# Performance work log

Hardware: AMD Instinct MI355X
Metric: run time of the kernel (lower is better)

## Reference

```python
import jax, jax.numpy as jnp
import numpy as np

KNN_K = 16
EPS = 1e-5


def _knn_idx(p, k):
    # p: [B,3,N] -> idx [B,N,k] of nearest neighbors (self excluded)
    pt = jnp.swapaxes(p, 1, 2)                      # [B,N,3]
    xx = jnp.sum(pt * pt, axis=-1)                  # [B,N]
    inner = jnp.einsum('bnd,bmd->bnm', pt, pt)      # [B,N,N]
    dist = -(xx[:, :, None] - 2.0 * inner + xx[:, None, :])  # -||pi-pj||^2
    N = pt.shape[1]
    dist = dist - 1e9 * jnp.eye(N, dtype=dist.dtype)
    return jax.lax.top_k(dist, k)[1]


def _ln(x, g, b):
    mu = jnp.mean(x, axis=-1, keepdims=True)
    var = jnp.mean((x - mu) ** 2, axis=-1, keepdims=True)
    return (x - mu) * jax.lax.rsqrt(var + EPS) * g + b


_gather = jax.vmap(lambda a, i: a[i])  # a:[N,C], i:[N,k] -> [N,k,C]


def setup_inputs() -> dict:
    key = jax.random.key(0)
    ks = jax.random.split(key, 24)
    Cin, C, B, N = 64, 128, 8, 2048
    s = lambda k_, shp, fan: jax.random.normal(k_, shp, jnp.float32) * (1.0 / np.sqrt(fan))
    return {
        'x': jax.random.normal(ks[0], (B, Cin, N), jnp.float32),
        'p': jax.random.normal(ks[1], (B, 3, N), jnp.float32),
        'Win': s(ks[2], (C, Cin), Cin), 'bin_': jnp.zeros((C,), jnp.float32),
        'Wq': s(ks[3], (C, C), C), 'Wk': s(ks[4], (C, C), C), 'Wv': s(ks[5], (C, C), C),
        'Wd1': s(ks[6], (C, 3), 3), 'bd1': jnp.zeros((C,), jnp.float32),
        'Wd2': s(ks[7], (C, C), C), 'bd2': jnp.zeros((C,), jnp.float32),
        'Wa': s(ks[8], (C, C), C), 'ba': jnp.zeros((C,), jnp.float32),
        'g1': jnp.ones((C,), jnp.float32), 'b1': jnp.zeros((C,), jnp.float32),
        'g2': jnp.ones((C,), jnp.float32), 'b2': jnp.zeros((C,), jnp.float32),
        'Wf1': s(ks[9], (4 * C, C), C), 'bf1': jnp.zeros((4 * C,), jnp.float32),
        'Wf2': s(ks[10], (C, 4 * C), 4 * C), 'bf2': jnp.zeros((C,), jnp.float32),
    }


def reference(x, p, Win, bin_, Wq, Wk, Wv, Wd1, bd1, Wd2, bd2, Wa, ba,
              g1, b1, g2, b2, Wf1, bf1, Wf2, bf2) -> jnp.ndarray:
    B, _, N = x.shape
    k = min(KNN_K, max(1, N - 1))
    # in_proj (conv1x1 == per-point linear); work in [B,N,C]
    h = jnp.einsum('oc,bcn->bno', Win, x) + bin_          # [B,N,C]
    hn = _ln(h, g1, b1)
    idx = _knn_idx(p, k)                                  # [B,N,k] (int)
    q = hn @ Wq.T                                         # [B,N,C]
    k_all = hn @ Wk.T
    v_all = hn @ Wv.T
    k_j = _gather(k_all, idx)                             # [B,N,k,C]
    v_j = _gather(v_all, idx)
    pt = jnp.swapaxes(p, 1, 2)                            # [B,N,3]
    p_j = _gather(pt, idx)                                # [B,N,k,3]
    rel = pt[:, :, None, :] - p_j                         # [B,N,k,3]
    d = jax.nn.relu(rel @ Wd1.T + bd1) @ Wd2.T + bd2      # [B,N,k,C]
    logits = (q[:, :, None, :] - k_j + d) @ Wa.T + ba     # [B,N,k,C]
    a = jax.nn.softmax(logits, axis=2)                    # softmax over neighbors
    y = jnp.sum(a * (v_j + d), axis=2)                    # [B,N,C]
    h = h + y
    h2 = _ln(h, g2, b2)
    h = h + jax.nn.relu(h2 @ Wf1.T + bf1) @ Wf2.T + bf2
    return jnp.swapaxes(h, 1, 2)                          # [B,C,N]
```

## Files before the change

### kernel.cpp

```cpp
#include <hip/hip_runtime.h>

typedef __bf16 bf16_t;
typedef __bf16 bf16x8 __attribute__((ext_vector_type(8)));
typedef __bf16 bf16x2 __attribute__((ext_vector_type(2)));
typedef float  f32x4  __attribute__((ext_vector_type(4)));

#define MFMA16(a,b,c) __builtin_amdgcn_mfma_f32_16x16x32_bf16((a),(b),(c),0,0,0)

#define BB 8
#define NN 2048
#define CC 128
#define CIN 64
#define KNB 16
#define BNT (BB*NN)

static __device__ __forceinline__ int remap256(int x) { return ((x & 7) << 5) | (x >> 3); }

static __device__ __forceinline__ bf16x8 cvt8(const float* src) {
  f32x4 a0 = *(const f32x4*)src;
  f32x4 a1 = *(const f32x4*)(src + 4);
  bf16x8 fr;
  fr[0] = (__bf16)a0[0]; fr[1] = (__bf16)a0[1]; fr[2] = (__bf16)a0[2]; fr[3] = (__bf16)a0[3];
  fr[4] = (__bf16)a1[0]; fr[5] = (__bf16)a1[1]; fr[6] = (__bf16)a1[2]; fr[7] = (__bf16)a1[3];
  return fr;
}

__global__ __launch_bounds__(256) void compw_k(
    const float* __restrict__ Wa, const float* __restrict__ Wq,
    const float* __restrict__ Wk, const float* __restrict__ Wd2,
    const float* __restrict__ ba, const float* __restrict__ bd2,
    float* __restrict__ Waq, float* __restrict__ Wak, float* __restrict__ Wda,
    float* __restrict__ cb) {
  __shared__ float Bs[64 * 128];
  int t = threadIdx.x;
  int mat = blockIdx.y;
  const float* B = mat == 0 ? Wq : mat == 1 ? Wk : Wd2;
  float* O = mat == 0 ? Waq : mat == 1 ? Wak : Wda;
  int row = blockIdx.x * 16 + (t >> 4);
  int c0 = (t & 15) * 8;
  const float* ar = Wa + row * 128;
  float acc[8] = {};
  for (int half = 0; half < 2; ++half) {
    __syncthreads();
    for (int i = t; i < 64 * 128 / 4; i += 256)
      ((f32x4*)Bs)[i] = ((const f32x4*)(B + half * 64 * 128))[i];
    __syncthreads();
    #pragma unroll 4
    for (int e = 0; e < 64; ++e) {
      float av = ar[half * 64 + e];
      #pragma unroll
      for (int j = 0; j < 8; ++j) acc[j] = fmaf(av, Bs[e * 128 + c0 + j], acc[j]);
    }
  }
  #pragma unroll
  for (int j = 0; j < 8; ++j) O[row * 128 + c0 + j] = acc[j];
  if (mat == 2 && blockIdx.x == 0 && t < 128) {
    float s = 0.f;
    for (int e = 0; e < 128; ++e) s = fmaf(Wa[t * 128 + e], bd2[e], s);
    cb[t] = ba[t] + s;
  }
}

__global__ __launch_bounds__(256) void inproj_ln_k(
    const float* __restrict__ x, const float* __restrict__ Win, const float* __restrict__ bin,
    const float* __restrict__ g1, const float* __restrict__ b1,
    float* __restrict__ h, bf16_t* __restrict__ hnb) {
  __shared__ bf16_t As[64 * 72];
  __shared__ bf16_t Bs[128 * 72];
  __shared__ float hs[64 * 132];
  int t = threadIdx.x;
  int lane = t & 63, w = t >> 6, quad = lane >> 4, l15 = lane & 15;
  int mBase = remap256(blockIdx.x) * 64;
  int b = mBase >> 11, n0 = mBase & (NN - 1);
  const float* xb = x + (size_t)b * CIN * NN;
  {
    int k = t >> 2, part = t & 3;
    #pragma unroll
    for (int i = 0; i < 4; ++i) {
      f32x4 v = *(const f32x4*)(xb + (size_t)k * NN + n0 + part * 16 + i * 4);
      #pragma unroll
      for (int j2 = 0; j2 < 4; ++j2) As[(part * 16 + i * 4 + j2) * 72 + k] = (__bf16)v[j2];
    }
  }
  {
    int row = t >> 1, seg = (t & 1) * 32;
    #pragma unroll
    for (int i = 0; i < 4; ++i)
      *(bf16x8*)(&Bs[row * 72 + seg + i * 8]) = cvt8(Win + (size_t)row * CIN + seg + i * 8);
  }
  __syncthreads();
  f32x4 acc[2][4] = {};
  #pragma unroll
  for (int s = 0; s < 2; ++s) {
    bf16x8 af[4];
    #pragma unroll
    for (int mt = 0; mt < 4; ++mt)
      af[mt] = *(const bf16x8*)(&As[(mt * 16 + l15) * 72 + s * 32 + quad * 8]);
    #pragma unroll
    for (int t2 = 0; t2 < 2; ++t2) {
      bf16x8 bfr = *(const bf16x8*)(&Bs[((w * 2 + t2) * 16 + l15) * 72 + s * 32 + quad * 8]);
      #pragma unroll
      for (int mt = 0; mt < 4; ++mt) acc[t2][mt] = MFMA16(af[mt], bfr, acc[t2][mt]);
    }
  }
  #pragma unroll
  for (int t2 = 0; t2 < 2; ++t2) {
    int col = (w * 2 + t2) * 16 + l15;
    float bv = bin[col];
    #pragma unroll
    for (int mt = 0; mt < 4; ++mt)
      #pragma unroll
      for (int reg = 0; reg < 4; ++reg)
        hs[(mt * 16 + quad * 4 + reg) * 132 + col] = acc[t2][mt][reg] + bv;
  }
  __syncthreads();
  {
    int row = t >> 2, c0 = (t & 3) * 32;
    float v[32];
    #pragma unroll
    for (int i = 0; i < 8; ++i) *(f32x4*)(v + i * 4) = *(const f32x4*)(&hs[row * 132 + c0 + i * 4]);
    float s1 = 0.f, s2 = 0.f;
    #pragma unroll
    for (int i = 0; i < 32; ++i) { s1 += v[i]; s2 += v[i] * v[i]; }
    s1 += __shfl_xor(s1, 1); s1 += __shfl_xor(s1, 2);
    s2 += __shfl_xor(s2, 1); s2 += __shfl_xor(s2, 2);
    float mu = s1 * (1.f / CC);
    float var = s2 * (1.f / CC) - mu * mu;
    float rs = rsqrtf(var + 1e-5f);
    float* hrow = h + (size_t)(mBase + row) * CC + c0;
    #pragma unroll
    for (int i = 0; i < 8; ++i) *(f32x4*)(hrow + i * 4) = *(const f32x4*)(v + i * 4);
    bf16_t* hnrow = hnb + (size_t)(mBase + row) * CC + c0;
    #pragma unroll
    for (int i = 0; i < 4; ++i) {
      f32x4 g4a = ((const f32x4*)g1)[(c0 >> 2) + i * 2],     g4b = ((const f32x4*)g1)[(c0 >> 2) + i * 2 + 1];
      f32x4 b4a = ((const f32x4*)b1)[(c0 >> 2) + i * 2],     b4b = ((const f32x4*)b1)[(c0 >> 2) + i * 2 + 1];
      bf16x8 o;
      #pragma unroll
      for (int j = 0; j < 4; ++j) o[j]     = (__bf16)((v[i * 8 + j]     - mu) * rs * g4a[j] + b4a[j]);
      #pragma unroll
      for (int j = 0; j < 4; ++j) o[4 + j] = (__bf16)((v[i * 8 + 4 + j] - mu) * rs * g4b[j] + b4b[j]);
      *(bf16x8*)(hnrow + i * 8) = o;
    }
  }
}

static __device__ __forceinline__ void cas(double& a, double& b) {
  double lo = fmin(a, b), hi = fmax(a, b); a = lo; b = hi;
}
#define S8(K,o) \
  cas(K[o+0],K[o+1]); cas(K[o+2],K[o+3]); cas(K[o+4],K[o+5]); cas(K[o+6],K[o+7]); \
  cas(K[o+0],K[o+2]); cas(K[o+1],K[o+3]); cas(K[o+4],K[o+6]); cas(K[o+5],K[o+7]); \
  cas(K[o+1],K[o+2]); cas(K[o+5],K[o+6]); \
  cas(K[o+0],K[o+4]); cas(K[o+1],K[o+5]); cas(K[o+2],K[o+6]); cas(K[o+3],K[o+7]); \
  cas(K[o+2],K[o+4]); cas(K[o+3],K[o+5]); \
  cas(K[o+1],K[o+2]); cas(K[o+3],K[o+4]); cas(K[o+5],K[o+6]);
#define M8(K,a,b) \
  K[a+0]=fmin(K[a+0],K[b+7]); K[a+1]=fmin(K[a+1],K[b+6]); K[a+2]=fmin(K[a+2],K[b+5]); K[a+3]=fmin(K[a+3],K[b+4]); \
  K[a+4]=fmin(K[a+4],K[b+3]); K[a+5]=fmin(K[a+5],K[b+2]); K[a+6]=fmin(K[a+6],K[b+1]); K[a+7]=fmin(K[a+7],K[b+0]); \
  cas(K[a+0],K[a+4]); cas(K[a+1],K[a+5]); cas(K[a+2],K[a+6]); cas(K[a+3],K[a+7]); \
  cas(K[a+0],K[a+2]); cas(K[a+1],K[a+3]); cas(K[a+4],K[a+6]); cas(K[a+5],K[a+7]); \
  cas(K[a+0],K[a+1]); cas(K[a+2],K[a+3]); cas(K[a+4],K[a+5]); cas(K[a+6],K[a+7]);

__global__ __launch_bounds__(256) void knn_k(const float* __restrict__ p, int* __restrict__ idxo) {
  __shared__ float px[NN], py[NN], pz[NN];
  int t = threadIdx.x;
  int b = blockIdx.x >> 9;
  int g = blockIdx.x & 511;
  const float* pb = p + (size_t)b * 3 * NN;
  for (int i = t; i < NN; i += 256) { px[i] = pb[i]; py[i] = pb[NN + i]; pz[i] = pb[2 * NN + i]; }
  __syncthreads();
  int w = t >> 6, lane = t & 63;
  int n = g * 4 + w;
  float pnx = px[n], pny = py[n], pnz = pz[n];
  double key[32];
  #pragma unroll
  for (int s = 0; s < 32; ++s) {
    int m = s * 64 + lane;
    float dx = pnx - px[m], dy = pny - py[m], dz = pnz - pz[m];
    float dist = dx * dx + dy * dy + dz * dz;
    unsigned db = (m == n) ? 0x7F800000u : __float_as_uint(dist);
    key[s] = __hiloint2double((int)db, m);
  }
  S8(key, 0); S8(key, 8); S8(key, 16); S8(key, 24);
  M8(key, 0, 8); M8(key, 16, 24); M8(key, 0, 16);
  const double DINF = __hiloint2double(0x7F900000, 0);
  int* myout = idxo + ((size_t)b * NN + n) * KNB;
  #pragma unroll 1
  for (int r = 0; r < 16; ++r) {
    double gm = key[0];
    #pragma unroll
    for (int off = 1; off < 64; off <<= 1) {
      double o = __shfl_xor(gm, off);
      gm = fmin(gm, o);
    }
    if (lane == 0) myout[r] = __double2loint(gm);
    bool win = (key[0] == gm);
    key[0] = win ? key[1] : key[0];
    key[1] = win ? key[2] : key[1];
    key[2] = win ? key[3] : key[2];
    key[3] = win ? key[4] : key[3];
    key[4] = win ? key[5] : key[4];
    key[5] = win ? key[6] : key[5];
    key[6] = win ? key[7] : key[6];
    key[7] = win ? DINF   : key[7];
  }
}

template<int EPI>
static __device__ __forceinline__ void gemm_body(
    const bf16_t* __restrict__ Ab,
    const float* __restrict__ W, const float* __restrict__ bias,
    float* __restrict__ outF, bf16_t* __restrict__ outB,
    const float* __restrict__ resid,
    int mBase, int nBase, int Ncol, int Kdim) {
  __shared__ bf16_t As[64 * 40];
  __shared__ bf16_t Bs[64 * 40];
  int t = threadIdx.x;
  int lane = t & 63, w = t >> 6, quad = lane >> 4, l15 = lane & 15;
  int r = t >> 2, seg = (t & 3) * 8;
  f32x4 acc[4] = {{0,0,0,0},{0,0,0,0},{0,0,0,0},{0,0,0,0}};
  for (int k0 = 0; k0 < Kdim; k0 += 32) {
    __syncthreads();
    *(bf16x8*)(&As[r * 40 + seg]) = *(const bf16x8*)(Ab + (size_t)(mBase + r) * Kdim + k0 + seg);
    *(bf16x8*)(&Bs[r * 40 + seg]) = cvt8(W + (size_t)(nBase + r) * Kdim + k0 + seg);
    __syncthreads();
    bf16x8 bfr = *(const bf16x8*)(&Bs[(w * 16 + l15) * 40 + quad * 8]);
    #pragma unroll
    for (int mt = 0; mt < 4; ++mt) {
      bf16x8 afr = *(const bf16x8*)(&As[(mt * 16 + l15) * 40 + quad * 8]);
      acc[mt] = MFMA16(afr, bfr, acc[mt]);
    }
  }
  int n = nBase + w * 16 + l15;
  float bv = bias ? bias[n] : 0.f;
  #pragma unroll
  for (int mt = 0; mt < 4; ++mt) {
    #pragma unroll
    for (int reg = 0; reg < 4; ++reg) {
      int m = mBase + mt * 16 + quad * 4 + reg;
      float val = acc[mt][reg] + bv;
      if (EPI == 0) {
        outF[(size_t)m * Ncol + n] = val;
      } else if (EPI == 1) {
        outB[(size_t)m * Ncol + n] = (__bf16)fmaxf(val, 0.f);
      } else if (EPI == 3) {
        outB[(size_t)m * Ncol + n] = (__bf16)val;
      } else {
        val += resid[(size_t)m * CC + n];
        int bo = m >> 11, np = m & (NN - 1);
        outF[((size_t)bo * CC + n) * NN + np] = val;
      }
    }
  }
}

template<int EPI>
__global__ __launch_bounds__(256) void gemm_k(
    const bf16_t* __restrict__ Ab,
    const float* __restrict__ W, const float* __restrict__ bias,
    float* __restrict__ outF, bf16_t* __restrict__ outB,
    const float* __restrict__ resid,
    int Ncol, int Kdim) {
  gemm_body<EPI>(Ab, W, bias, outF, outB, resid, remap256(blockIdx.x) * 64, blockIdx.y * 64, Ncol, Kdim);
}

__global__ __launch_bounds__(256) void gemm_qkv_k(
    const bf16_t* __restrict__ hnb,
    const float* __restrict__ Waq, const float* __restrict__ Wak, const float* __restrict__ Wv,
    float* __restrict__ qa, bf16_t* __restrict__ ka, bf16_t* __restrict__ vb) {
  int sel = blockIdx.y >> 1;
  int nB = (blockIdx.y & 1) * 64, mB = remap256(blockIdx.x) * 64;
  if (sel == 0)      gemm_body<0>(hnb, Waq, nullptr, qa, nullptr, nullptr, mB, nB, CC, CC);
  else if (sel == 1) gemm_body<3>(hnb, Wak, nullptr, nullptr, ka, nullptr, mB, nB, CC, CC);
  else               gemm_body<3>(hnb, Wv, nullptr, nullptr, vb, nullptr, mB, nB, CC, CC);
}

__global__ __launch_bounds__(256, 3) void attn_k(
    const float* __restrict__ qabuf, const bf16_t* __restrict__ kabuf, const bf16_t* __restrict__ vbuf,
    const float* __restrict__ p, const int* __restrict__ idx,
    const float* __restrict__ Wd1, const float* __restrict__ bd1,
    const float* __restrict__ Wd2, const float* __restrict__ Wda,
    const float* __restrict__ cb, const float* __restrict__ bd2,
    const float* __restrict__ g2, const float* __restrict__ b2,
    const float* __restrict__ h, float* __restrict__ hres, bf16_t* __restrict__ h2) {
  __shared__ f32x4 wd1s[128];
  __shared__ f32x4 rels4[64];
  __shared__ int idxs[64];
  __shared__ float hrs[4 * 128];
  int t = threadIdx.x;
  int lane = t & 63, w = t >> 6, quad = lane >> 4, l15 = lane & 15;
  int batch = blockIdx.x & 7, grp = blockIdx.x >> 3;
  int bn0 = batch * NN + grp * 4;
  const float* pb = p + (size_t)batch * 3 * NN;
  int col0 = w * 32 + l15;
  int col1 = col0 + 16;

  bf16x8 Bd[2][4], Bl[2][4];
  #pragma unroll
  for (int t2 = 0; t2 < 2; ++t2) {
    int row = w * 32 + t2 * 16 + l15;
    #pragma unroll
    for (int s = 0; s < 4; ++s) {
      Bd[t2][s] = cvt8(Wd2 + (size_t)row * CC + s * 32 + quad * 8);
      Bl[t2][s] = cvt8(Wda + (size_t)row * CC + s * 32 + quad * 8);
    }
  }

  if (t < 64) {
    int jj = idx[(size_t)bn0 * KNB + t];
    idxs[t] = jj;
    int npt = grp * 4 + (t >> 4);
    f32x4 rv;
    rv[0] = pb[npt]          - pb[jj];
    rv[1] = pb[NN + npt]     - pb[NN + jj];
    rv[2] = pb[2 * NN + npt] - pb[2 * NN + jj];
    rv[3] = 0.f;
    rels4[t] = rv;
  }
  if (t < 128) {
    f32x4 wv;
    wv[0] = Wd1[t * 3]; wv[1] = Wd1[t * 3 + 1]; wv[2] = Wd1[t * 3 + 2]; wv[3] = bd1[t];
    wd1s[t] = wv;
  }
  __syncthreads();

  f32x4 relv[4];
  #pragma unroll
  for (int mt = 0; mt < 4; ++mt) relv[mt] = rels4[mt * 16 + l15];
  f32x4 accd[2][4] = {};
  f32x4 accl[2][4] = {};
  #pragma unroll
  for (int s = 0; s < 4; ++s) {
    bf16x8 af[4];
    #pragma unroll
    for (int j = 0; j < 8; ++j) {
      f32x4 wv = wd1s[s * 32 + quad * 8 + j];
      #pragma unroll
      for (int mt = 0; mt < 4; ++mt) {
        float tv = fmaf(wv[0], relv[mt][0], fmaf(wv[1], relv[mt][1], fmaf(wv[2], relv[mt][2], wv[3])));
        af[mt][j] = (__bf16)fmaxf(tv, 0.f);
      }
    }
    #pragma unroll
    for (int t2 = 0; t2 < 2; ++t2)
      #pragma unroll
      for (int mt = 0; mt < 4; ++mt) {
        accd[t2][mt] = MFMA16(af[mt], Bd[t2][s], accd[t2][mt]);
        accl[t2][mt] = MFMA16(af[mt], Bl[t2][s], accl[t2][mt]);
      }
  }

  float qv[2][4];
  #pragma unroll
  for (int mt = 0; mt < 4; ++mt) {
    qv[0][mt] = qabuf[(size_t)(bn0 + mt) * CC + col0];
    qv[1][mt] = qabuf[(size_t)(bn0 + mt) * CC + col1];
  }
  float kav[2][4][4], vv[2][4][4];
  #pragma unroll
  for (int mt = 0; mt < 4; ++mt)
    #pragma unroll
    for (int reg = 0; reg < 4; ++reg) {
      size_t base = (size_t)(batch * NN + idxs[mt * 16 + quad * 4 + reg]) * CC;
      kav[0][mt][reg] = (float)kabuf[base + col0];
      kav[1][mt][reg] = (float)kabuf[base + col1];
      vv[0][mt][reg]  = (float)vbuf[base + col0];
      vv[1][mt][reg]  = (float)vbuf[base + col1];
    }
  float hv[2][4];
  if (quad == 0) {
    #pragma unroll
    for (int mt = 0; mt < 4; ++mt) {
      hv[0][mt] = h[(size_t)(bn0 + mt) * CC + col0];
      hv[1][mt] = h[(size_t)(bn0 + mt) * CC + col1];
    }
  }

  #pragma unroll
  for (int t2 = 0; t2 < 2; ++t2) {
    int col = t2 ? col1 : col0;
    float cbv = cb[col];
    float b2v = bd2[col];
    #pragma unroll
    for (int mt = 0; mt < 4; ++mt) {
      float qc = qv[t2][mt] + cbv;
      float lv0 = qc - kav[t2][mt][0] + accl[t2][mt][0];
      float lv1 = qc - kav[t2][mt][1] + accl[t2][mt][1];
      float lv2 = qc - kav[t2][mt][2] + accl[t2][mt][2];
      float lv3 = qc - kav[t2][mt][3] + accl[t2][mt][3];
      float mx = fmaxf(fmaxf(lv0, lv1), fmaxf(lv2, lv3));
      mx = fmaxf(mx, __shfl_xor(mx, 16));
      mx = fmaxf(mx, __shfl_xor(mx, 32));
      float e0 = __expf(lv0 - mx), e1 = __expf(lv1 - mx);
      float e2 = __expf(lv2 - mx), e3 = __expf(lv3 - mx);
      float ss = e0 + e1 + e2 + e3;
      ss += __shfl_xor(ss, 16); ss += __shfl_xor(ss, 32);
      float yv = e0 * (vv[t2][mt][0] + accd[t2][mt][0] + b2v)
               + e1 * (vv[t2][mt][1] + accd[t2][mt][1] + b2v)
               + e2 * (vv[t2][mt][2] + accd[t2][mt][2] + b2v)
               + e3 * (vv[t2][mt][3] + accd[t2][mt][3] + b2v);
      yv += __shfl_xor(yv, 16); yv += __shfl_xor(yv, 32);
      if (quad == 0) {
        float hvv = hv[t2][mt] + yv / ss;
        hres[(size_t)(bn0 + mt) * CC + col] = hvv;
        hrs[mt * 128 + col] = hvv;
      }
    }
  }
  __syncthreads();

  {
    int c0 = lane * 2;
    float v0 = hrs[w * 128 + c0], v1 = hrs[w * 128 + c0 + 1];
    float s1 = v0 + v1, s2 = v0 * v0 + v1 * v1;
    #pragma unroll
    for (int off = 1; off < 64; off <<= 1) { s1 += __shfl_xor(s1, off); s2 += __shfl_xor(s2, off); }
    float mu = s1 * (1.f / CC);
    float var = s2 * (1.f / CC) - mu * mu;
    float rs = rsqrtf(var + 1e-5f);
    bf16x2 o;
    o[0] = (__bf16)((v0 - mu) * rs * g2[c0] + b2[c0]);
    o[1] = (__bf16)((v1 - mu) * rs * g2[c0 + 1] + b2[c0 + 1]);
    *(bf16x2*)(h2 + (size_t)(bn0 + w) * CC + c0) = o;
  }
}

extern "C" void kernel_launch(void* const* d_in, const int* in_sizes, int n_in,
                              void* d_out, int out_size, void* d_ws, size_t ws_size,
                              hipStream_t stream) {
  const float* x   = (const float*)d_in[0];
  const float* p   = (const float*)d_in[1];
  const float* Win = (const float*)d_in[2];
  const float* bin = (const float*)d_in[3];
  const float* Wq  = (const float*)d_in[4];
  const float* Wk  = (const float*)d_in[5];
  const float* Wv  = (const float*)d_in[6];
  const float* Wd1 = (const float*)d_in[7];
  const float* bd1 = (const float*)d_in[8];
  const float* Wd2 = (const float*)d_in[9];
  const float* bd2 = (const float*)d_in[10];
  const float* Wa  = (const float*)d_in[11];
  const float* ba  = (const float*)d_in[12];
  const float* g1  = (const float*)d_in[13];
  const float* b1  = (const float*)d_in[14];
  const float* g2  = (const float*)d_in[15];
  const float* b2  = (const float*)d_in[16];
  const float* Wf1 = (const float*)d_in[17];
  const float* bf1 = (const float*)d_in[18];
  const float* Wf2 = (const float*)d_in[19];
  const float* bf2 = (const float*)d_in[20];
  float* out = (float*)d_out;

  const size_t SZ = (size_t)BNT * CC;
  float* wsf = (float*)d_ws;
  float*  h    = wsf;
  bf16_t* hnb  = (bf16_t*)(wsf + SZ);
  float*  hres = wsf + SZ;
  float*  qa   = wsf + 2 * SZ;
  bf16_t* kab  = (bf16_t*)(wsf + 3 * SZ);
  bf16_t* vb   = kab + SZ;
  bf16_t* g    = (bf16_t*)(wsf + 2 * SZ);
  bf16_t* h2   = (bf16_t*)(wsf + 4 * SZ);
  int*    idxw = (int*)(wsf + 4 * SZ + SZ / 2);
  float*  Waq  = wsf + 4 * SZ + SZ / 2 + (size_t)BNT * KNB;
  float*  Wak  = Waq + 16384;
  float*  Wda  = Wak + 16384;
  float*  cbv  = Wda + 16384;

  compw_k<<<dim3(8, 3), 256, 0, stream>>>(Wa, Wq, Wk, Wd2, ba, bd2, Waq, Wak, Wda, cbv);
  inproj_ln_k<<<BNT / 64, 256, 0, stream>>>(x, Win, bin, g1, b1, h, hnb);
  knn_k<<<BB * (NN / 4), 256, 0, stream>>>(p, idxw);
  gemm_qkv_k<<<dim3(BNT / 64, 6), 256, 0, stream>>>(hnb, Waq, Wak, Wv, qa, kab, vb);
  attn_k<<<BNT / 4, 256, 0, stream>>>(qa, kab, vb, p, idxw, Wd1, bd1, Wd2, Wda, cbv, bd2,
                                      g2, b2, h, hres, h2);
  gemm_k<1><<<dim3(BNT / 64, 8), 256, 0, stream>>>(h2, Wf1, bf1, nullptr, g, nullptr, 4 * CC, CC);
  gemm_k<2><<<dim3(BNT / 64, 2), 256, 0, stream>>>(g, Wf2, bf2, out, nullptr, hres, CC, 4 * CC);
}
```

Baseline: 312.2 us.

## Use 128x128 bf16 GEMM tiles with direct global-to-LDS loads and prequantized weights

```diff
diff --git a/kernel.cpp b/kernel.cpp
--- a/kernel.cpp
+++ b/kernel.cpp
@@ -15,6 +15,7 @@
 #define BNT (BB*NN)
 
 static __device__ __forceinline__ int remap256(int x) { return ((x & 7) << 5) | (x >> 3); }
+static __device__ __forceinline__ int remap128(int x) { return ((x & 7) << 4) | (x >> 3); }
 
 static __device__ __forceinline__ bf16x8 cvt8(const float* src) {
   f32x4 a0 = *(const f32x4*)src;
@@ -25,17 +26,32 @@
   return fr;
 }
 
+static __device__ __forceinline__ void gload_lds16(const bf16_t* g, bf16_t* l) {
+  __builtin_amdgcn_global_load_lds(
+      (const __attribute__((address_space(1))) unsigned int*)g,
+      (__attribute__((address_space(3))) unsigned int*)l, 16, 0, 0);
+}
+
 __global__ __launch_bounds__(256) void compw_k(
     const float* __restrict__ Wa, const float* __restrict__ Wq,
     const float* __restrict__ Wk, const float* __restrict__ Wd2,
     const float* __restrict__ ba, const float* __restrict__ bd2,
-    float* __restrict__ Waq, float* __restrict__ Wak, float* __restrict__ Wda,
-    float* __restrict__ cb) {
+    const float* __restrict__ Wv, const float* __restrict__ Wf1, const float* __restrict__ Wf2,
+    bf16_t* __restrict__ Wqkvb, bf16_t* __restrict__ Wdab, float* __restrict__ cb,
+    bf16_t* __restrict__ Wf1b, bf16_t* __restrict__ Wf2b) {
   __shared__ float Bs[64 * 128];
   int t = threadIdx.x;
   int mat = blockIdx.y;
+  if (mat >= 3) {
+    int nel = (mat == 3) ? 16384 : 65536;
+    const float* S = mat == 3 ? Wv : (mat == 4 ? Wf1 : Wf2);
+    bf16_t* D = mat == 3 ? (Wqkvb + 256 * 128) : (mat == 4 ? Wf1b : Wf2b);
+    for (int i = blockIdx.x * 256 + t; i * 8 < nel; i += 2048)
+      *(bf16x8*)(D + i * 8) = cvt8(S + i * 8);
+    return;
+  }
   const float* B = mat == 0 ? Wq : mat == 1 ? Wk : Wd2;
-  float* O = mat == 0 ? Waq : mat == 1 ? Wak : Wda;
+  bf16_t* O = mat == 0 ? Wqkvb : mat == 1 ? (Wqkvb + 128 * 128) : Wdab;
   int row = blockIdx.x * 16 + (t >> 4);
   int c0 = (t & 15) * 8;
   const float* ar = Wa + row * 128;
@@ -53,7 +69,7 @@
     }
   }
   #pragma unroll
-  for (int j = 0; j < 8; ++j) O[row * 128 + c0 + j] = acc[j];
+  for (int j = 0; j < 8; ++j) O[row * 128 + c0 + j] = (__bf16)acc[j];
   if (mat == 2 && blockIdx.x == 0 && t < 128) {
     float s = 0.f;
     for (int e = 0; e < 128; ++e) s = fmaf(Wa[t * 128 + e], bd2[e], s);
@@ -208,79 +224,83 @@
 }
 
 template<int EPI>
-static __device__ __forceinline__ void gemm_body(
-    const bf16_t* __restrict__ Ab,
-    const float* __restrict__ W, const float* __restrict__ bias,
-    float* __restrict__ outF, bf16_t* __restrict__ outB,
-    const float* __restrict__ resid,
+static __device__ __forceinline__ void gemm128_body(
+    const bf16_t* __restrict__ A, const bf16_t* __restrict__ Wb, const float* __restrict__ bias,
+    float* __restrict__ outF, bf16_t* __restrict__ outB, const float* __restrict__ resid,
     int mBase, int nBase, int Ncol, int Kdim) {
-  __shared__ bf16_t As[64 * 40];
-  __shared__ bf16_t Bs[64 * 40];
+  __shared__ bf16_t As[128 * 32];
+  __shared__ bf16_t Bs[128 * 32];
   int t = threadIdx.x;
   int lane = t & 63, w = t >> 6, quad = lane >> 4, l15 = lane & 15;
-  int r = t >> 2, seg = (t & 3) * 8;
-  f32x4 acc[4] = {{0,0,0,0},{0,0,0,0},{0,0,0,0},{0,0,0,0}};
+  int wm = (w & 1) * 64, wn = (w >> 1) * 64;
+  int srow = lane >> 2, scol = (lane & 3) * 8;
+  f32x4 acc[4][4] = {};
   for (int k0 = 0; k0 < Kdim; k0 += 32) {
     __syncthreads();
-    *(bf16x8*)(&As[r * 40 + seg]) = *(const bf16x8*)(Ab + (size_t)(mBase + r) * Kdim + k0 + seg);
-    *(bf16x8*)(&Bs[r * 40 + seg]) = cvt8(W + (size_t)(nBase + r) * Kdim + k0 + seg);
+    #pragma unroll
+    for (int i = 0; i < 2; ++i) {
+      int rbase = w * 32 + i * 16;
+      gload_lds16(A  + (size_t)(mBase + rbase + srow) * Kdim + k0 + scol, &As[rbase * 32]);
+      gload_lds16(Wb + (size_t)(nBase + rbase + srow) * Kdim + k0 + scol, &Bs[rbase * 32]);
+    }
     __syncthreads();
-    bf16x8 bfr = *(const bf16x8*)(&Bs[(w * 16 + l15) * 40 + quad * 8]);
+    bf16x8 af[4], bf[4];
+    #pragma unroll
+    for (int mt = 0; mt < 4; ++mt) af[mt] = *(const bf16x8*)(&As[(wm + mt * 16 + l15) * 32 + quad * 8]);
+    #pragma unroll
+    for (int nt = 0; nt < 4; ++nt) bf[nt] = *(const bf16x8*)(&Bs[(wn + nt * 16 + l15) * 32 + quad * 8]);
+    #pragma unroll
+    for (int mt = 0; mt < 4; ++mt)
+      #pragma unroll
+      for (int nt = 0; nt < 4; ++nt)
+        acc[mt][nt] = MFMA16(af[mt], bf[nt], acc[mt][nt]);
+  }
+  #pragma unroll
+  for (int nt = 0; nt < 4; ++nt) {
+    int n = nBase + wn + nt * 16 + l15;
+    float bv = bias ? bias[n] : 0.f;
     #pragma unroll
     for (int mt = 0; mt < 4; ++mt) {
-      bf16x8 afr = *(const bf16x8*)(&As[(mt * 16 + l15) * 40 + quad * 8]);
-      acc[mt] = MFMA16(afr, bfr, acc[mt]);
-    }
-  }
-  int n = nBase + w * 16 + l15;
-  float bv = bias ? bias[n] : 0.f;
-  #pragma unroll
-  for (int mt = 0; mt < 4; ++mt) {
-    #pragma unroll
-    for (int reg = 0; reg < 4; ++reg) {
-      int m = mBase + mt * 16 + quad * 4 + reg;
-      float val = acc[mt][reg] + bv;
-      if (EPI == 0) {
-        outF[(size_t)m * Ncol + n] = val;
-      } else if (EPI == 1) {
-        outB[(size_t)m * Ncol + n] = (__bf16)fmaxf(val, 0.f);
-      } else if (EPI == 3) {
-        outB[(size_t)m * Ncol + n] = (__bf16)val;
-      } else {
-        val += resid[(size_t)m * CC + n];
-        int bo = m >> 11, np = m & (NN - 1);
-        outF[((size_t)bo * CC + n) * NN + np] = val;
+      #pragma unroll
+      for (int reg = 0; reg < 4; ++reg) {
+        int m = mBase + wm + mt * 16 + quad * 4 + reg;
+        float val = acc[mt][nt][reg] + bv;
+        if (EPI == 1) {
+          outB[(size_t)m * Ncol + n] = (__bf16)fmaxf(val, 0.f);
+        } else if (EPI == 3) {
+          outB[(size_t)m * Ncol + n] = (__bf16)val;
+        } else {
+          val += resid[(size_t)m * CC + n];
+          int bo = m >> 11, np = m & (NN - 1);
+          outF[((size_t)bo * CC + n) * NN + np] = val;
+        }
       }
     }
   }
 }
 
 template<int EPI>
-__global__ __launch_bounds__(256) void gemm_k(
-    const bf16_t* __restrict__ Ab,
-    const float* __restrict__ W, const float* __restrict__ bias,
-    float* __restrict__ outF, bf16_t* __restrict__ outB,
-    const float* __restrict__ resid,
+__global__ __launch_bounds__(256) void gemm128_k(
+    const bf16_t* __restrict__ A, const bf16_t* __restrict__ Wb, const float* __restrict__ bias,
+    float* __restrict__ outF, bf16_t* __restrict__ outB, const float* __restrict__ resid,
     int Ncol, int Kdim) {
-  gemm_body<EPI>(Ab, W, bias, outF, outB, resid, remap256(blockIdx.x) * 64, blockIdx.y * 64, Ncol, Kdim);
+  gemm128_body<EPI>(A, Wb, bias, outF, outB, resid,
+                    remap128(blockIdx.x) * 128, blockIdx.y * 128, Ncol, Kdim);
 }
 
 __global__ __launch_bounds__(256) void gemm_qkv_k(
-    const bf16_t* __restrict__ hnb,
-    const float* __restrict__ Waq, const float* __restrict__ Wak, const float* __restrict__ Wv,
-    float* __restrict__ qa, bf16_t* __restrict__ ka, bf16_t* __restrict__ vb) {
-  int sel = blockIdx.y >> 1;
-  int nB = (blockIdx.y & 1) * 64, mB = remap256(blockIdx.x) * 64;
-  if (sel == 0)      gemm_body<0>(hnb, Waq, nullptr, qa, nullptr, nullptr, mB, nB, CC, CC);
-  else if (sel == 1) gemm_body<3>(hnb, Wak, nullptr, nullptr, ka, nullptr, mB, nB, CC, CC);
-  else               gemm_body<3>(hnb, Wv, nullptr, nullptr, vb, nullptr, mB, nB, CC, CC);
+    const bf16_t* __restrict__ hnb, const bf16_t* __restrict__ Wqkvb, bf16_t* __restrict__ qkv) {
+  int y = blockIdx.y;
+  gemm128_body<3>(hnb, Wqkvb + (size_t)y * 128 * CC, nullptr, nullptr,
+                  qkv + (size_t)y * BNT * CC, nullptr,
+                  remap128(blockIdx.x) * 128, 0, CC, CC);
 }
 
 __global__ __launch_bounds__(256, 3) void attn_k(
-    const float* __restrict__ qabuf, const bf16_t* __restrict__ kabuf, const bf16_t* __restrict__ vbuf,
+    const bf16_t* __restrict__ qabuf, const bf16_t* __restrict__ kabuf, const bf16_t* __restrict__ vbuf,
     const float* __restrict__ p, const int* __restrict__ idx,
     const float* __restrict__ Wd1, const float* __restrict__ bd1,
-    const float* __restrict__ Wd2, const float* __restrict__ Wda,
+    const float* __restrict__ Wd2, const bf16_t* __restrict__ Wdab,
     const float* __restrict__ cb, const float* __restrict__ bd2,
     const float* __restrict__ g2, const float* __restrict__ b2,
     const float* __restrict__ h, float* __restrict__ hres, bf16_t* __restrict__ h2) {
@@ -303,7 +323,7 @@
     #pragma unroll
     for (int s = 0; s < 4; ++s) {
       Bd[t2][s] = cvt8(Wd2 + (size_t)row * CC + s * 32 + quad * 8);
-      Bl[t2][s] = cvt8(Wda + (size_t)row * CC + s * 32 + quad * 8);
+      Bl[t2][s] = *(const bf16x8*)(Wdab + (size_t)row * CC + s * 32 + quad * 8);
     }
   }
 
@@ -325,37 +345,11 @@
   }
   __syncthreads();
 
-  f32x4 relv[4];
-  #pragma unroll
-  for (int mt = 0; mt < 4; ++mt) relv[mt] = rels4[mt * 16 + l15];
-  f32x4 accd[2][4] = {};
-  f32x4 accl[2][4] = {};
-  #pragma unroll
-  for (int s = 0; s < 4; ++s) {
-    bf16x8 af[4];
-    #pragma unroll
-    for (int j = 0; j < 8; ++j) {
-      f32x4 wv = wd1s[s * 32 + quad * 8 + j];
-      #pragma unroll
-      for (int mt = 0; mt < 4; ++mt) {
-        float tv = fmaf(wv[0], relv[mt][0], fmaf(wv[1], relv[mt][1], fmaf(wv[2], relv[mt][2], wv[3])));
-        af[mt][j] = (__bf16)fmaxf(tv, 0.f);
-      }
-    }
-    #pragma unroll
-    for (int t2 = 0; t2 < 2; ++t2)
-      #pragma unroll
-      for (int mt = 0; mt < 4; ++mt) {
-        accd[t2][mt] = MFMA16(af[mt], Bd[t2][s], accd[t2][mt]);
-        accl[t2][mt] = MFMA16(af[mt], Bl[t2][s], accl[t2][mt]);
-      }
-  }
-
   float qv[2][4];
   #pragma unroll
   for (int mt = 0; mt < 4; ++mt) {
-    qv[0][mt] = qabuf[(size_t)(bn0 + mt) * CC + col0];
-    qv[1][mt] = qabuf[(size_t)(bn0 + mt) * CC + col1];
+    qv[0][mt] = (float)qabuf[(size_t)(bn0 + mt) * CC + col0];
+    qv[1][mt] = (float)qabuf[(size_t)(bn0 + mt) * CC + col1];
   }
   float kav[2][4][4], vv[2][4][4];
   #pragma unroll
@@ -375,6 +369,32 @@
       hv[0][mt] = h[(size_t)(bn0 + mt) * CC + col0];
       hv[1][mt] = h[(size_t)(bn0 + mt) * CC + col1];
     }
+  }
+
+  f32x4 relv[4];
+  #pragma unroll
+  for (int mt = 0; mt < 4; ++mt) relv[mt] = rels4[mt * 16 + l15];
+  f32x4 accd[2][4] = {};
+  f32x4 accl[2][4] = {};
+  #pragma unroll
+  for (int s = 0; s < 4; ++s) {
+    bf16x8 af[4];
+    #pragma unroll
+    for (int j = 0; j < 8; ++j) {
+      f32x4 wv = wd1s[s * 32 + quad * 8 + j];
+      #pragma unroll
+      for (int mt = 0; mt < 4; ++mt) {
+        float tv = fmaf(wv[0], relv[mt][0], fmaf(wv[1], relv[mt][1], fmaf(wv[2], relv[mt][2], wv[3])));
+        af[mt][j] = (__bf16)fmaxf(tv, 0.f);
+      }
+    }
+    #pragma unroll
+    for (int t2 = 0; t2 < 2; ++t2)
+      #pragma unroll
+      for (int mt = 0; mt < 4; ++mt) {
+        accd[t2][mt] = MFMA16(af[mt], Bd[t2][s], accd[t2][mt]);
+        accl[t2][mt] = MFMA16(af[mt], Bl[t2][s], accl[t2][mt]);
+      }
   }
 
   #pragma unroll
@@ -457,23 +477,24 @@
   float*  h    = wsf;
   bf16_t* hnb  = (bf16_t*)(wsf + SZ);
   float*  hres = wsf + SZ;
-  float*  qa   = wsf + 2 * SZ;
-  bf16_t* kab  = (bf16_t*)(wsf + 3 * SZ);
-  bf16_t* vb   = kab + SZ;
+  bf16_t* qkv  = (bf16_t*)(wsf + 2 * SZ);
   bf16_t* g    = (bf16_t*)(wsf + 2 * SZ);
   bf16_t* h2   = (bf16_t*)(wsf + 4 * SZ);
   int*    idxw = (int*)(wsf + 4 * SZ + SZ / 2);
-  float*  Waq  = wsf + 4 * SZ + SZ / 2 + (size_t)BNT * KNB;
-  float*  Wak  = Waq + 16384;
-  float*  Wda  = Wak + 16384;
-  float*  cbv  = Wda + 16384;
-
-  compw_k<<<dim3(8, 3), 256, 0, stream>>>(Wa, Wq, Wk, Wd2, ba, bd2, Waq, Wak, Wda, cbv);
+  bf16_t* Wqkvb = (bf16_t*)(wsf + 4 * SZ + SZ / 2 + SZ / 8);
+  bf16_t* Wdab  = Wqkvb + 384 * 128;
+  bf16_t* Wf1b  = Wdab + 128 * 128;
+  bf16_t* Wf2b  = Wf1b + 512 * 128;
+  float*  cbv   = (float*)(Wf2b + 128 * 512);
+
+  compw_k<<<dim3(8, 6), 256, 0, stream>>>(Wa, Wq, Wk, Wd2, ba, bd2, Wv, Wf1, Wf2,
+                                          Wqkvb, Wdab, cbv, Wf1b, Wf2b);
   inproj_ln_k<<<BNT / 64, 256, 0, stream>>>(x, Win, bin, g1, b1, h, hnb);
   knn_k<<<BB * (NN / 4), 256, 0, stream>>>(p, idxw);
-  gemm_qkv_k<<<dim3(BNT / 64, 6), 256, 0, stream>>>(hnb, Waq, Wak, Wv, qa, kab, vb);
-  attn_k<<<BNT / 4, 256, 0, stream>>>(qa, kab, vb, p, idxw, Wd1, bd1, Wd2, Wda, cbv, bd2,
+  gemm_qkv_k<<<dim3(BNT / 128, 3), 256, 0, stream>>>(hnb, Wqkvb, qkv);
+  attn_k<<<BNT / 4, 256, 0, stream>>>(qkv, qkv + SZ, qkv + 2 * SZ, p, idxw,
+                                      Wd1, bd1, Wd2, Wdab, cbv, bd2,
                                       g2, b2, h, hres, h2);
-  gemm_k<1><<<dim3(BNT / 64, 8), 256, 0, stream>>>(h2, Wf1, bf1, nullptr, g, nullptr, 4 * CC, CC);
-  gemm_k<2><<<dim3(BNT / 64, 2), 256, 0, stream>>>(g, Wf2, bf2, out, nullptr, hres, CC, 4 * CC);
-}
+  gemm128_k<1><<<dim3(BNT / 128, 4), 256, 0, stream>>>(h2, Wf1b, bf1, nullptr, g, nullptr, 4 * CC, CC);
+  gemm128_k<2><<<dim3(BNT / 128, 1), 256, 0, stream>>>(g, Wf2b, bf2, out, nullptr, hres, CC, 4 * CC);
+}
```

After: 433.2 us. +38.7%, slower.
